# Kernel optimization log

Measured on AMD Instinct MI355X. Metric: run time of the kernel, lower is better.

## Reference

```python
import jax, jax.numpy as jnp
import numpy as np

B, E, C, M, H = 4, 8, 512, 1024, 4096

def setup_inputs() -> dict:
    key = jax.random.key(0)
    k1, k2, k3, k4, k5 = jax.random.split(key, 5)
    s = 1.0 / np.sqrt(M)
    return {
        "x": jax.random.normal(k1, (B, E, C, M), dtype=jnp.float32),
        "fc1_weight": jax.random.normal(k2, (E, H, M), dtype=jnp.float32) * s,
        "fc1_bias": jax.random.normal(k3, (E, 1, H), dtype=jnp.float32) * 0.02,
        "fc2_weight": jax.random.normal(k4, (E, H, M), dtype=jnp.float32) * (1.0 / np.sqrt(H)),
        "fc2_bias": jax.random.normal(k5, (E, 1, M), dtype=jnp.float32) * 0.02,
    }

def reference(x, fc1_weight, fc1_bias, fc2_weight, fc2_bias):
    # x: [B, E, C, M] -> [E, B*C, M]
    b, e, c, m = x.shape
    xe = jnp.transpose(x, (1, 0, 2, 3)).reshape(e, b * c, m)
    # fc1: [E,T,M] @ [E,M,H] (fp32 grouped GEMM with bias)
    h = jnp.einsum('etm,ehm->eth', xe.astype(jnp.float32), fc1_weight.astype(jnp.float32)) + fc1_bias.astype(jnp.float32)
    h = jax.nn.relu(h)
    # fc2: [E,T,H] @ [E,H,M] + bias (dropout is identity)
    o = jnp.einsum('eth,ehm->etm', h, fc2_weight) + fc2_bias
    o = o.reshape(e, b, c, m)
    return jnp.transpose(o, (1, 0, 2, 3))
```

## Files before the change

kernel.cpp:

```cpp
#include <hip/hip_runtime.h>
#include <hip/hip_bf16.h>

typedef __bf16 bf16x8 __attribute__((ext_vector_type(8)));
typedef __bf16 bf16x4 __attribute__((ext_vector_type(4)));
typedef float  f32x4  __attribute__((ext_vector_type(4)));

constexpr int Ee = 8, Cc = 512, Mm = 1024, Hh = 4096, Tt = 2048;

__device__ __forceinline__ void async16(void* lds, const void* g) {
  __builtin_amdgcn_global_load_lds(
      (const __attribute__((address_space(1))) void*)g,
      (__attribute__((address_space(3))) void*)lds, 16, 0, 0);
}

#define FENCE() asm volatile("" ::: "memory")
#define BARRIER() do { FENCE(); __builtin_amdgcn_s_barrier(); FENCE(); } while (0)

__device__ __forceinline__ int xcd_swz(int id, int n) {
  const int q = n >> 3, r = n & 7;
  const int x = id & 7, k = id >> 3;
  return (x < r ? x * (q + 1) : r * (q + 1) + (x - r) * q) + k;
}

__device__ __forceinline__ void gemm256(
    const __bf16* __restrict__ aT, const __bf16* __restrict__ bT, const int K,
    __bf16 (*Ab)[2][128][64], __bf16 (*Bb)[2][128][64],
    f32x4 (&acc)[8][4]) {
  const int tid = threadIdx.x;
  const int lane = tid & 63, wid = tid >> 6;
  const int wr = wid >> 2, wcn = wid & 3;
  const int l8 = lane >> 3;
  const int colSwzE = (((lane & 7) ^ l8) << 3);
  const int NT = K >> 6;

  int pblk[2];
  pblk[0] = (lane >> 4) ^ (lane & 7);
  pblk[1] = (4 + (lane >> 4)) ^ (lane & 7);

  bf16x8 aF[8][2];
  bf16x8 bF[2][2];

  auto STAGE = [&](int s, int u) {
    if (s >= NT) return;
    const int d = s & 1;
    if (u < 2) {
      const __bf16* src = aT + (size_t)(u * 128 + wid * 16 + l8) * K + s * 64 + colSwzE;
#pragma unroll
      for (int i = 0; i < 2; ++i)
        async16(&Ab[d][u][wid * 16 + i * 8][0], src + (size_t)(i * 8) * K);
    } else {
      const __bf16* src = bT + (size_t)((u - 2) * 128 + wid * 16 + l8) * K + s * 64 + colSwzE;
#pragma unroll
      for (int i = 0; i < 2; ++i)
        async16(&Bb[d][u - 2][wid * 16 + i * 8][0], src + (size_t)(i * 8) * K);
    }
  };

  STAGE(0, 0); STAGE(0, 1); STAGE(0, 2); STAGE(0, 3);
  STAGE(1, 0); STAGE(1, 1);
  asm volatile("s_waitcnt vmcnt(4)" ::: "memory");
  BARRIER();

  for (int t = 0; t < NT; ++t) {
    const int d = t & 1;
    const char* pa = (const char*)&Ab[d][wr][0][0];
    const char* pb = (const char*)&Bb[d][wcn >> 1][0][0];
    const int brow = (wcn & 1) * 64;

    STAGE(t + 1, 2); STAGE(t + 1, 3);

#pragma unroll
    for (int mi = 0; mi < 8; ++mi)
#pragma unroll
      for (int kh = 0; kh < 2; ++kh)
        aF[mi][kh] = *(const bf16x8*)(pa + (mi * 16 + (lane & 15)) * 128 + pblk[kh] * 16);
#pragma unroll
    for (int ni = 0; ni < 2; ++ni)
#pragma unroll
      for (int kh = 0; kh < 2; ++kh)
        bF[ni][kh] = *(const bf16x8*)(pb + (brow + ni * 16 + (lane & 15)) * 128 + pblk[kh] * 16);

    BARRIER();

    STAGE(t + 2, 0); STAGE(t + 2, 1);

    __builtin_amdgcn_s_setprio(1);
#pragma unroll
    for (int mi = 0; mi < 8; ++mi)
#pragma unroll
      for (int ni = 0; ni < 2; ++ni)
#pragma unroll
        for (int kh = 0; kh < 2; ++kh)
          acc[mi][ni] = __builtin_amdgcn_mfma_f32_16x16x32_bf16(bF[ni][kh], aF[mi][kh], acc[mi][ni], 0, 0, 0);
    __builtin_amdgcn_s_setprio(0);

#pragma unroll
    for (int ni = 0; ni < 2; ++ni)
#pragma unroll
      for (int kh = 0; kh < 2; ++kh)
        bF[ni][kh] = *(const bf16x8*)(pb + (brow + (2 + ni) * 16 + (lane & 15)) * 128 + pblk[kh] * 16);

    __builtin_amdgcn_s_setprio(1);
#pragma unroll
    for (int mi = 0; mi < 8; ++mi)
#pragma unroll
      for (int ni = 0; ni < 2; ++ni)
#pragma unroll
        for (int kh = 0; kh < 2; ++kh)
          acc[mi][2 + ni] = __builtin_amdgcn_mfma_f32_16x16x32_bf16(bF[ni][kh], aF[mi][kh], acc[mi][2 + ni], 0, 0, 0);
    __builtin_amdgcn_s_setprio(0);

    if (t < NT - 2) { asm volatile("s_waitcnt vmcnt(4)" ::: "memory"); }
    else            { asm volatile("s_waitcnt vmcnt(0)" ::: "memory"); }
    BARRIER();
  }
}

__global__ __launch_bounds__(512, 2) void fc1g_kernel(
    const __bf16* __restrict__ xb, int eOffA,
    const __bf16* __restrict__ w1b, int eOffB,
    const float* __restrict__ b1, __bf16* __restrict__ hb,
    int e0, int t_base, int tcap, int nbT) {
  __shared__ __bf16 Ab[2][2][128][64];
  __shared__ __bf16 Bb[2][2][128][64];
  const int nbN = Hh / 256;
  const int id = xcd_swz(blockIdx.x, gridDim.x);
  const int z = id / (nbN * nbT);
  const int rm = id % (nbN * nbT);
  const int tblk = (rm % nbT) * 256, nblk = (rm / nbT) * 256;
  const int lane = threadIdx.x & 63, wid = threadIdx.x >> 6;
  const int wr = wid >> 2, wcn = wid & 3;

  const __bf16* aT = xb + ((size_t)(eOffA + z) * Tt + t_base + tblk) * Mm;
  const __bf16* bT = w1b + ((size_t)(eOffB + z) * Hh + nblk) * Mm;

  f32x4 acc[8][4];
#pragma unroll
  for (int i = 0; i < 8; ++i)
#pragma unroll
    for (int j = 0; j < 4; ++j) acc[i][j] = (f32x4){0.f, 0.f, 0.f, 0.f};

  gemm256(aT, bT, Mm, Ab, Bb, acc);

  const float* bias = b1 + (size_t)(e0 + z) * Hh;
#pragma unroll
  for (int ni = 0; ni < 4; ++ni) {
    const int n0 = nblk + wcn * 64 + ni * 16 + ((lane >> 4) << 2);
    const f32x4 b4 = *(const f32x4*)(bias + n0);
#pragma unroll
    for (int mi = 0; mi < 8; ++mi) {
      const int trow = tblk + wr * 128 + mi * 16 + (lane & 15);
      f32x4 v = acc[mi][ni];
      bf16x4 o;
#pragma unroll
      for (int rr = 0; rr < 4; ++rr) {
        float f = v[rr] + b4[rr];
        o[rr] = (__bf16)(f > 0.f ? f : 0.f);
      }
      *(bf16x4*)(hb + ((size_t)z * tcap + trow) * Hh + n0) = o;
    }
  }
}

__global__ __launch_bounds__(512, 2) void fc2g_kernel(
    const __bf16* __restrict__ hb, int tcap,
    const __bf16* __restrict__ w2t, int eOffB,
    const float* __restrict__ b2, float* __restrict__ out,
    int e0, int t_base, int nbT) {
  __shared__ __bf16 Ab[2][2][128][64];
  __shared__ __bf16 Bb[2][2][128][64];
  const int nbN = Mm / 256;
  const int id = xcd_swz(blockIdx.x, gridDim.x);
  const int z = id / (nbN * nbT);
  const int rm = id % (nbN * nbT);
  const int tblk = (rm % nbT) * 256, nblk = (rm / nbT) * 256;
  const int lane = threadIdx.x & 63, wid = threadIdx.x >> 6;
  const int wr = wid >> 2, wcn = wid & 3;
  const int e = e0 + z;

  const __bf16* aT = hb + ((size_t)z * tcap + tblk) * Hh;
  const __bf16* bT = w2t + ((size_t)(eOffB + z) * Mm + nblk) * Hh;

  f32x4 acc[8][4];
#pragma unroll
  for (int i = 0; i < 8; ++i)
#pragma unroll
    for (int j = 0; j < 4; ++j) acc[i][j] = (f32x4){0.f, 0.f, 0.f, 0.f};

  gemm256(aT, bT, Hh, Ab, Bb, acc);

  const float* bias = b2 + (size_t)e * Mm;
#pragma unroll
  for (int ni = 0; ni < 4; ++ni) {
    const int m0 = nblk + wcn * 64 + ni * 16 + ((lane >> 4) << 2);
    const f32x4 b4 = *(const f32x4*)(bias + m0);
#pragma unroll
    for (int mi = 0; mi < 8; ++mi) {
      const int t = t_base + tblk + wr * 128 + mi * 16 + (lane & 15);
      const int bb = t >> 9, cc = t & 511;
      f32x4 v = acc[mi][ni];
#pragma unroll
      for (int rr = 0; rr < 4; ++rr) v[rr] += b4[rr];
      *(f32x4*)(out + ((((size_t)bb * Ee + e) * Cc + cc) << 10) + m0) = v;
    }
  }
}

__global__ __launch_bounds__(256) void prep_all_kernel(
    const float* __restrict__ x, const float* __restrict__ w1,
    const float* __restrict__ w2, __bf16* __restrict__ xb,
    __bf16* __restrict__ w1b, __bf16* __restrict__ w2t) {
  __shared__ __bf16 tile[64][68];
  const int bid = blockIdx.x;
  if (bid < 8192) {
    size_t idx8 = (size_t)bid * 256 + threadIdx.x;
    int m8 = (int)(idx8 & 127);
    int t = (int)((idx8 >> 7) & 2047);
    int z = (int)(idx8 >> 18);
    int b = t >> 9, c = t & 511;
    const float* src = x + ((((size_t)b * Ee + z) * Cc + c) << 10) + (m8 << 3);
    f32x4 v0 = *(const f32x4*)src;
    f32x4 v1 = *(const f32x4*)(src + 4);
    bf16x8 o;
    o[0] = (__bf16)v0[0]; o[1] = (__bf16)v0[1]; o[2] = (__bf16)v0[2]; o[3] = (__bf16)v0[3];
    o[4] = (__bf16)v1[0]; o[5] = (__bf16)v1[1]; o[6] = (__bf16)v1[2]; o[7] = (__bf16)v1[3];
    *(bf16x8*)(xb + (idx8 << 3)) = o;
  } else if (bid < 24576) {
    size_t i8 = (size_t)(bid - 8192) * 256 + threadIdx.x;
    const float* src = w1 + (i8 << 3);
    f32x4 v0 = *(const f32x4*)src;
    f32x4 v1 = *(const f32x4*)(src + 4);
    bf16x8 o;
    o[0] = (__bf16)v0[0]; o[1] = (__bf16)v0[1]; o[2] = (__bf16)v0[2]; o[3] = (__bf16)v0[3];
    o[4] = (__bf16)v1[0]; o[5] = (__bf16)v1[1]; o[6] = (__bf16)v1[2]; o[7] = (__bf16)v1[3];
    *(bf16x8*)(w1b + (i8 << 3)) = o;
  } else {
    const int tb = bid - 24576;
    const int z = tb >> 10;
    const int rem = tb & 1023;
    const int m0 = (rem & 15) * 64;
    const int h0 = (rem >> 4) * 64;
    const int tid = threadIdx.x;
    const int cg = tid & 15, rg = tid >> 4;
#pragma unroll
    for (int p = 0; p < 4; ++p) {
      int hl = rg + p * 16;
      f32x4 v = *(const f32x4*)(w2 + (((size_t)z * Hh + h0 + hl) << 10) + m0 + (cg << 2));
#pragma unroll
      for (int i = 0; i < 4; ++i) tile[(cg << 2) + i][hl] = (__bf16)v[i];
    }
    __syncthreads();
#pragma unroll
    for (int p = 0; p < 4; ++p) {
      int ml = rg + p * 16;
      uint2 pk = *(const uint2*)(&tile[ml][cg << 2]);
      *(uint2*)(w2t + ((size_t)z * Mm + m0 + ml) * Hh + h0 + (cg << 2)) = pk;
    }
  }
}

__global__ __launch_bounds__(256) void cvt_x_kernel(
    const float* __restrict__ x, __bf16* __restrict__ xb, int e0) {
  size_t idx8 = (size_t)blockIdx.x * 256 + threadIdx.x;
  int m8 = (int)(idx8 & 127);
  int t = (int)((idx8 >> 7) & 2047);
  int z = (int)(idx8 >> 18);
  int b = t >> 9, c = t & 511, e = e0 + z;
  const float* src = x + ((((size_t)b * Ee + e) * Cc + c) << 10) + (m8 << 3);
  f32x4 v0 = *(const f32x4*)src;
  f32x4 v1 = *(const f32x4*)(src + 4);
  bf16x8 o;
  o[0] = (__bf16)v0[0]; o[1] = (__bf16)v0[1]; o[2] = (__bf16)v0[2]; o[3] = (__bf16)v0[3];
  o[4] = (__bf16)v1[0]; o[5] = (__bf16)v1[1]; o[6] = (__bf16)v1[2]; o[7] = (__bf16)v1[3];
  *(bf16x8*)(xb + (idx8 << 3)) = o;
}

__global__ __launch_bounds__(256) void cvt_lin_kernel(
    const float* __restrict__ in, __bf16* __restrict__ outb) {
  size_t i8 = (size_t)blockIdx.x * 256 + threadIdx.x;
  const float* src = in + (i8 << 3);
  f32x4 v0 = *(const f32x4*)src;
  f32x4 v1 = *(const f32x4*)(src + 4);
  bf16x8 o;
  o[0] = (__bf16)v0[0]; o[1] = (__bf16)v0[1]; o[2] = (__bf16)v0[2]; o[3] = (__bf16)v0[3];
  o[4] = (__bf16)v1[0]; o[5] = (__bf16)v1[1]; o[6] = (__bf16)v1[2]; o[7] = (__bf16)v1[3];
  *(bf16x8*)(outb + (i8 << 3)) = o;
}

__global__ __launch_bounds__(256) void tr_w2_kernel(
    const float* __restrict__ w2, __bf16* __restrict__ w2t, int e0) {
  __shared__ __bf16 tile[64][68];
  const int z = blockIdx.z, e = e0 + z;
  const int m0 = blockIdx.x * 64, h0 = blockIdx.y * 64;
  const int tid = threadIdx.x;
  const int cg = tid & 15, rg = tid >> 4;
#pragma unroll
  for (int p = 0; p < 4; ++p) {
    int hl = rg + p * 16;
    f32x4 v = *(const f32x4*)(w2 + (((size_t)e * Hh + h0 + hl) << 10) + m0 + (cg << 2));
#pragma unroll
    for (int i = 0; i < 4; ++i) tile[(cg << 2) + i][hl] = (__bf16)v[i];
  }
  __syncthreads();
#pragma unroll
  for (int p = 0; p < 4; ++p) {
    int ml = rg + p * 16;
    uint2 pk = *(const uint2*)(&tile[ml][cg << 2]);
    *(uint2*)(w2t + ((size_t)z * Mm + m0 + ml) * Hh + h0 + (cg << 2)) = pk;
  }
}

extern "C" void kernel_launch(void* const* d_in, const int* in_sizes, int n_in,
                              void* d_out, int out_size, void* d_ws, size_t ws_size,
                              hipStream_t stream) {
  const float* x  = (const float*)d_in[0];
  const float* w1 = (const float*)d_in[1];
  const float* b1 = (const float*)d_in[2];
  const float* w2 = (const float*)d_in[3];
  const float* b2 = (const float*)d_in[4];
  float* out = (float*)d_out;

  const size_t xbS = (size_t)Tt * Mm * 2;
  const size_t w1S = (size_t)Hh * Mm * 2;
  const size_t w2S = (size_t)Mm * Hh * 2;
  const size_t hbS = (size_t)Tt * Hh * 2;
  char* ws = (char*)d_ws;

  if (ws_size >= Ee * (xbS + w1S + w2S + hbS)) {
    __bf16* xb  = (__bf16*)ws;
    __bf16* w1b = (__bf16*)(ws + Ee * xbS);
    __bf16* w2t = (__bf16*)(ws + Ee * (xbS + w1S));
    __bf16* hb  = (__bf16*)(ws + Ee * (xbS + w1S + w2S));
    prep_all_kernel<<<32768, 256, 0, stream>>>(x, w1, w2, xb, w1b, w2t);
    fc1g_kernel<<<(Hh / 256) * (Tt / 256) * Ee, 512, 0, stream>>>(xb, 0, w1b, 0, b1, hb, 0, 0, Tt, Tt / 256);
    fc2g_kernel<<<(Mm / 256) * (Tt / 256) * Ee, 512, 0, stream>>>(hb, Tt, w2t, 0, b2, out, 0, 0, Tt / 256);
  } else if (ws_size >= Ee * (xbS + w1S + w2S) + hbS) {
    __bf16* xb  = (__bf16*)ws;
    __bf16* w1b = (__bf16*)(ws + Ee * xbS);
    __bf16* w2t = (__bf16*)(ws + Ee * (xbS + w1S));
    __bf16* hb  = (__bf16*)(ws + Ee * (xbS + w1S + w2S));
    int Gh = (int)((ws_size - Ee * (xbS + w1S + w2S)) / hbS);
    if (Gh > Ee) Gh = Ee;
    prep_all_kernel<<<32768, 256, 0, stream>>>(x, w1, w2, xb, w1b, w2t);
    for (int e0 = 0; e0 < Ee; e0 += Gh) {
      int g = (Ee - e0) < Gh ? (Ee - e0) : Gh;
      fc1g_kernel<<<(Hh / 256) * (Tt / 256) * g, 512, 0, stream>>>(xb, e0, w1b, e0, b1, hb, e0, 0, Tt, Tt / 256);
      fc2g_kernel<<<(Mm / 256) * (Tt / 256) * g, 512, 0, stream>>>(hb, Tt, w2t, e0, b2, out, e0, 0, Tt / 256);
    }
  } else if (ws_size >= xbS + w1S + w2S + hbS) {
    int G = (int)(ws_size / (xbS + w1S + w2S + hbS));
    if (G > Ee) G = Ee;
    __bf16* xb  = (__bf16*)ws;
    __bf16* w1b = (__bf16*)(ws + (size_t)G * xbS);
    __bf16* w2t = (__bf16*)(ws + (size_t)G * (xbS + w1S));
    __bf16* hb  = (__bf16*)(ws + (size_t)G * (xbS + w1S + w2S));
    for (int e0 = 0; e0 < Ee; e0 += G) {
      int g = (Ee - e0) < G ? (Ee - e0) : G;
      cvt_x_kernel<<<g * 1024, 256, 0, stream>>>(x, xb, e0);
      cvt_lin_kernel<<<g * 2048, 256, 0, stream>>>(w1 + (size_t)e0 * Hh * Mm, w1b);
      tr_w2_kernel<<<dim3(Mm / 64, Hh / 64, g), 256, 0, stream>>>(w2, w2t, e0);
      fc1g_kernel<<<(Hh / 256) * (Tt / 256) * g, 512, 0, stream>>>(xb, 0, w1b, 0, b1, hb, e0, 0, Tt, Tt / 256);
      fc2g_kernel<<<(Mm / 256) * (Tt / 256) * g, 512, 0, stream>>>(hb, Tt, w2t, 0, b2, out, e0, 0, Tt / 256);
    }
  } else {
    __bf16* xb  = (__bf16*)ws;
    __bf16* w1b = (__bf16*)(ws + xbS);
    __bf16* w2t = (__bf16*)(ws + xbS + w1S);
    __bf16* hb  = (__bf16*)(ws + xbS + w1S + w2S);
    size_t rem = ws_size > (xbS + w1S + w2S) ? ws_size - (xbS + w1S + w2S) : 0;
    int Tc = (int)(rem / ((size_t)Hh * 2)) & ~255;
    if (Tc > Tt) Tc = Tt;
    if (Tc < 256) Tc = 256;
    for (int e0 = 0; e0 < Ee; ++e0) {
      cvt_x_kernel<<<1024, 256, 0, stream>>>(x, xb, e0);
      cvt_lin_kernel<<<2048, 256, 0, stream>>>(w1 + (size_t)e0 * Hh * Mm, w1b);
      tr_w2_kernel<<<dim3(Mm / 64, Hh / 64, 1), 256, 0, stream>>>(w2, w2t, e0);
      for (int t0 = 0; t0 < Tt; t0 += Tc) {
        int tc = (Tt - t0) < Tc ? (Tt - t0) : Tc;
        fc1g_kernel<<<(Hh / 256) * (tc / 256), 512, 0, stream>>>(xb, 0, w1b, 0, b1, hb, e0, t0, Tc, tc / 256);
        fc2g_kernel<<<(Mm / 256) * (tc / 256), 512, 0, stream>>>(hb, Tc, w2t, 0, b2, out, e0, t0, tc / 256);
      }
    }
  }
}
```

Measured before the change: 488.0 us.

## Make fc1 blocks persistent over four N-tiles, prefetching next tile during epilogue

Adds fc1p_kernel, in which each block handles four consecutive 256-wide H tiles for one token block. The GEMM is split into prologue and body so the next tile's first loads are issued before the bias/ReLU/store epilogue of the current tile, hiding the pipeline fill. The grid shrinks from 512 to 256 blocks, which matches 256 CUs at one wave but loses the second resident block per CU. fc1g and fc2g also change their tile index order so neighbouring blocks share the token tile instead of the weight tile.

```diff
diff --git a/kernel.cpp b/kernel.cpp
--- a/kernel.cpp
+++ b/kernel.cpp
@@ -22,17 +22,46 @@
   return (x < r ? x * (q + 1) : r * (q + 1) + (x - r) * q) + k;
 }
 
-__device__ __forceinline__ void gemm256(
+#define GEOM_LOCALS \
+  const int tid = threadIdx.x; \
+  const int lane = tid & 63, wid = tid >> 6; \
+  const int l8 = lane >> 3; \
+  const int colSwzE = (((lane & 7) ^ l8) << 3); \
+  const int NT = K >> 6;
+
+#define STAGE_IMPL \
+  auto STAGE = [&](int s, int u) { \
+    if (s >= NT) return; \
+    const int d = s & 1; \
+    if (u < 2) { \
+      const __bf16* src = aT + (size_t)(u * 128 + wid * 16 + l8) * K + s * 64 + colSwzE; \
+      _Pragma("unroll") \
+      for (int i = 0; i < 2; ++i) \
+        async16(&Ab[d][u][wid * 16 + i * 8][0], src + (size_t)(i * 8) * K); \
+    } else { \
+      const __bf16* src = bT + (size_t)((u - 2) * 128 + wid * 16 + l8) * K + s * 64 + colSwzE; \
+      _Pragma("unroll") \
+      for (int i = 0; i < 2; ++i) \
+        async16(&Bb[d][u - 2][wid * 16 + i * 8][0], src + (size_t)(i * 8) * K); \
+    } \
+  };
+
+__device__ __forceinline__ void gemm_pro(
+    const __bf16* __restrict__ aT, const __bf16* __restrict__ bT, const int K,
+    __bf16 (*Ab)[2][128][64], __bf16 (*Bb)[2][128][64]) {
+  GEOM_LOCALS
+  STAGE_IMPL
+  STAGE(0, 0); STAGE(0, 1); STAGE(0, 2); STAGE(0, 3);
+  STAGE(1, 0); STAGE(1, 1);
+}
+
+__device__ __forceinline__ void gemm_body(
     const __bf16* __restrict__ aT, const __bf16* __restrict__ bT, const int K,
     __bf16 (*Ab)[2][128][64], __bf16 (*Bb)[2][128][64],
     f32x4 (&acc)[8][4]) {
-  const int tid = threadIdx.x;
-  const int lane = tid & 63, wid = tid >> 6;
+  GEOM_LOCALS
+  STAGE_IMPL
   const int wr = wid >> 2, wcn = wid & 3;
-  const int l8 = lane >> 3;
-  const int colSwzE = (((lane & 7) ^ l8) << 3);
-  const int NT = K >> 6;
-
   int pblk[2];
   pblk[0] = (lane >> 4) ^ (lane & 7);
   pblk[1] = (4 + (lane >> 4)) ^ (lane & 7);
@@ -40,24 +69,6 @@
   bf16x8 aF[8][2];
   bf16x8 bF[2][2];
 
-  auto STAGE = [&](int s, int u) {
-    if (s >= NT) return;
-    const int d = s & 1;
-    if (u < 2) {
-      const __bf16* src = aT + (size_t)(u * 128 + wid * 16 + l8) * K + s * 64 + colSwzE;
-#pragma unroll
-      for (int i = 0; i < 2; ++i)
-        async16(&Ab[d][u][wid * 16 + i * 8][0], src + (size_t)(i * 8) * K);
-    } else {
-      const __bf16* src = bT + (size_t)((u - 2) * 128 + wid * 16 + l8) * K + s * 64 + colSwzE;
-#pragma unroll
-      for (int i = 0; i < 2; ++i)
-        async16(&Bb[d][u - 2][wid * 16 + i * 8][0], src + (size_t)(i * 8) * K);
-    }
-  };
-
-  STAGE(0, 0); STAGE(0, 1); STAGE(0, 2); STAGE(0, 3);
-  STAGE(1, 0); STAGE(1, 1);
   asm volatile("s_waitcnt vmcnt(4)" ::: "memory");
   BARRIER();
 
@@ -113,6 +124,63 @@
     if (t < NT - 2) { asm volatile("s_waitcnt vmcnt(4)" ::: "memory"); }
     else            { asm volatile("s_waitcnt vmcnt(0)" ::: "memory"); }
     BARRIER();
+  }
+}
+
+__global__ __launch_bounds__(512, 2) void fc1p_kernel(
+    const __bf16* __restrict__ xb, int eOffA,
+    const __bf16* __restrict__ w1b, int eOffB,
+    const float* __restrict__ b1, __bf16* __restrict__ hb,
+    int e0, int tcap) {
+  __shared__ __bf16 Ab[2][2][128][64];
+  __shared__ __bf16 Bb[2][2][128][64];
+  const int id = xcd_swz(blockIdx.x, gridDim.x);
+  const int z = id >> 5;
+  const int rm = id & 31;
+  const int ngrp = rm & 3;
+  const int tblk = (rm >> 2) * 256;
+  const int lane = threadIdx.x & 63, wid = threadIdx.x >> 6;
+  const int wr = wid >> 2, wcn = wid & 3;
+
+  const __bf16* aT = xb + ((size_t)(eOffA + z) * Tt + tblk) * Mm;
+  const float* bias = b1 + (size_t)(e0 + z) * Hh;
+
+  const __bf16* bT = w1b + ((size_t)(eOffB + z) * Hh + (ngrp * 4 + 0) * 256) * Mm;
+  gemm_pro(aT, bT, Mm, Ab, Bb);
+
+#pragma unroll 1
+  for (int i = 0; i < 4; ++i) {
+    const int nblk = (ngrp * 4 + i) * 256;
+    f32x4 acc[8][4];
+#pragma unroll
+    for (int a = 0; a < 8; ++a)
+#pragma unroll
+      for (int b = 0; b < 4; ++b) acc[a][b] = (f32x4){0.f, 0.f, 0.f, 0.f};
+
+    gemm_body(aT, bT, Mm, Ab, Bb, acc);
+
+    if (i < 3) {
+      bT = w1b + ((size_t)(eOffB + z) * Hh + (ngrp * 4 + i + 1) * 256) * Mm;
+      gemm_pro(aT, bT, Mm, Ab, Bb);
+    }
+
+#pragma unroll
+    for (int ni = 0; ni < 4; ++ni) {
+      const int n0 = nblk + wcn * 64 + ni * 16 + ((lane >> 4) << 2);
+      const f32x4 b4 = *(const f32x4*)(bias + n0);
+#pragma unroll
+      for (int mi = 0; mi < 8; ++mi) {
+        const int trow = tblk + wr * 128 + mi * 16 + (lane & 15);
+        f32x4 v = acc[mi][ni];
+        bf16x4 o;
+#pragma unroll
+        for (int rr = 0; rr < 4; ++rr) {
+          float f = v[rr] + b4[rr];
+          o[rr] = (__bf16)(f > 0.f ? f : 0.f);
+        }
+        *(bf16x4*)(hb + ((size_t)z * tcap + trow) * Hh + n0) = o;
+      }
+    }
   }
 }
 
@@ -127,7 +195,7 @@
   const int id = xcd_swz(blockIdx.x, gridDim.x);
   const int z = id / (nbN * nbT);
   const int rm = id % (nbN * nbT);
-  const int tblk = (rm % nbT) * 256, nblk = (rm / nbT) * 256;
+  const int tblk = (rm / nbN) * 256, nblk = (rm % nbN) * 256;
   const int lane = threadIdx.x & 63, wid = threadIdx.x >> 6;
   const int wr = wid >> 2, wcn = wid & 3;
 
@@ -140,7 +208,8 @@
 #pragma unroll
     for (int j = 0; j < 4; ++j) acc[i][j] = (f32x4){0.f, 0.f, 0.f, 0.f};
 
-  gemm256(aT, bT, Mm, Ab, Bb, acc);
+  gemm_pro(aT, bT, Mm, Ab, Bb);
+  gemm_body(aT, bT, Mm, Ab, Bb, acc);
 
   const float* bias = b1 + (size_t)(e0 + z) * Hh;
 #pragma unroll
@@ -173,7 +242,7 @@
   const int id = xcd_swz(blockIdx.x, gridDim.x);
   const int z = id / (nbN * nbT);
   const int rm = id % (nbN * nbT);
-  const int tblk = (rm % nbT) * 256, nblk = (rm / nbT) * 256;
+  const int tblk = (rm / nbN) * 256, nblk = (rm % nbN) * 256;
   const int lane = threadIdx.x & 63, wid = threadIdx.x >> 6;
   const int wr = wid >> 2, wcn = wid & 3;
   const int e = e0 + z;
@@ -187,7 +256,8 @@
 #pragma unroll
     for (int j = 0; j < 4; ++j) acc[i][j] = (f32x4){0.f, 0.f, 0.f, 0.f};
 
-  gemm256(aT, bT, Hh, Ab, Bb, acc);
+  gemm_pro(aT, bT, Hh, Ab, Bb);
+  gemm_body(aT, bT, Hh, Ab, Bb, acc);
 
   const float* bias = b2 + (size_t)e * Mm;
 #pragma unroll
@@ -332,7 +402,7 @@
     __bf16* w2t = (__bf16*)(ws + Ee * (xbS + w1S));
     __bf16* hb  = (__bf16*)(ws + Ee * (xbS + w1S + w2S));
     prep_all_kernel<<<32768, 256, 0, stream>>>(x, w1, w2, xb, w1b, w2t);
-    fc1g_kernel<<<(Hh / 256) * (Tt / 256) * Ee, 512, 0, stream>>>(xb, 0, w1b, 0, b1, hb, 0, 0, Tt, Tt / 256);
+    fc1p_kernel<<<32 * Ee, 512, 0, stream>>>(xb, 0, w1b, 0, b1, hb, 0, Tt);
     fc2g_kernel<<<(Mm / 256) * (Tt / 256) * Ee, 512, 0, stream>>>(hb, Tt, w2t, 0, b2, out, 0, 0, Tt / 256);
   } else if (ws_size >= Ee * (xbS + w1S + w2S) + hbS) {
     __bf16* xb  = (__bf16*)ws;
@@ -344,7 +414,7 @@
     prep_all_kernel<<<32768, 256, 0, stream>>>(x, w1, w2, xb, w1b, w2t);
     for (int e0 = 0; e0 < Ee; e0 += Gh) {
       int g = (Ee - e0) < Gh ? (Ee - e0) : Gh;
-      fc1g_kernel<<<(Hh / 256) * (Tt / 256) * g, 512, 0, stream>>>(xb, e0, w1b, e0, b1, hb, e0, 0, Tt, Tt / 256);
+      fc1p_kernel<<<32 * g, 512, 0, stream>>>(xb, e0, w1b, e0, b1, hb, e0, Tt);
       fc2g_kernel<<<(Mm / 256) * (Tt / 256) * g, 512, 0, stream>>>(hb, Tt, w2t, e0, b2, out, e0, 0, Tt / 256);
     }
   } else if (ws_size >= xbS + w1S + w2S + hbS) {
@@ -359,7 +429,7 @@
       cvt_x_kernel<<<g * 1024, 256, 0, stream>>>(x, xb, e0);
       cvt_lin_kernel<<<g * 2048, 256, 0, stream>>>(w1 + (size_t)e0 * Hh * Mm, w1b);
       tr_w2_kernel<<<dim3(Mm / 64, Hh / 64, g), 256, 0, stream>>>(w2, w2t, e0);
-      fc1g_kernel<<<(Hh / 256) * (Tt / 256) * g, 512, 0, stream>>>(xb, 0, w1b, 0, b1, hb, e0, 0, Tt, Tt / 256);
+      fc1p_kernel<<<32 * g, 512, 0, stream>>>(xb, 0, w1b, 0, b1, hb, e0, Tt);
       fc2g_kernel<<<(Mm / 256) * (Tt / 256) * g, 512, 0, stream>>>(hb, Tt, w2t, 0, b2, out, e0, 0, Tt / 256);
     }
   } else {
```

After: 460.0 us. 1.06x faster.
